# Kernel tuning notes

Hardware: AMD Instinct MI355X
Metric: run time of the kernel (lower is better)

Reference implementation:

```python
import jax, jax.numpy as jnp
import numpy as np

BN_EPS = 1e-5


def setup_inputs() -> dict:
    key = jax.random.key(0)
    ks = jax.random.split(key, 6)
    N, C, T, V = 64, 64, 300, 25
    num_A, O = 3, 64
    x = jax.random.normal(ks[0], (N, C, T, V), dtype=jnp.float32)
    A = jax.random.uniform(ks[1], (num_A, V, V), dtype=jnp.float32)
    # 1x1 conv weights per adjacency branch: W[a, o, c], bias b[a, o]
    W = jax.random.normal(ks[2], (num_A, O, C), dtype=jnp.float32) * (1.0 / np.sqrt(C))
    b = jax.random.normal(ks[3], (num_A, O), dtype=jnp.float32) * 0.01
    gamma = jnp.ones((O,), dtype=jnp.float32)
    beta = jnp.zeros((O,), dtype=jnp.float32)
    return {"x": x, "A": A, "W": W, "b": b, "gamma": gamma, "beta": beta}


def reference(x, A, W, b, gamma, beta):
    # x: [N, C, T, V]; A: [num_A, V, V]; W: [num_A, O, C]; b: [num_A, O]
    # For each branch a: xa = x @ A_a over the joint dim V, then a 1x1 conv
    # (channel mix W_a + bias b_a), accumulated over branches.
    z = jnp.einsum('nctv,avw->anctw', x, A)          # [num_A, N, C, T, V]
    y = jnp.einsum('anctw,aoc->notw', z, W)          # [N, O, T, V]
    y = y + jnp.sum(b, axis=0)[None, :, None, None]
    # BatchNorm2d (training mode: batch statistics over N, T, V per channel)
    mean = jnp.mean(y, axis=(0, 2, 3), keepdims=True)
    var = jnp.mean((y - mean) ** 2, axis=(0, 2, 3), keepdims=True)
    y = (y - mean) * jax.lax.rsqrt(var + BN_EPS)
    y = y * gamma[None, :, None, None] + beta[None, :, None, None]
    return jax.nn.relu(y)
```

## Files before the change

### kernel.cpp

```cpp
#include <hip/hip_runtime.h>


typedef __attribute__((ext_vector_type(8))) short short8;
typedef __attribute__((ext_vector_type(4))) float f32x4;

static __device__ __forceinline__ float bf2f(unsigned short u) {
    return __uint_as_float(((unsigned)u) << 16);
}
static __device__ __forceinline__ unsigned short f2bf(float f) {
    unsigned u = __float_as_uint(f);
    u += 0x7FFFu + ((u >> 16) & 1u);
    return (unsigned short)(u >> 16);
}

#define MFMA16(a, b, c) __builtin_amdgcn_mfma_f32_16x16x32_bf16((a), (b), (c), 0, 0, 0)

__global__ __launch_bounds__(256, 4)
void gcn_k1(const void* __restrict__ xg, const void* __restrict__ Ag,
            const void* __restrict__ Wg, const void* __restrict__ gammag,
            float* __restrict__ gstats, unsigned short* __restrict__ y_ws)
{
    const int tid  = threadIdx.x;
    const int wv   = tid >> 6;
    const int lane = tid & 63;
    const int n16  = lane & 15;
    const int kg   = lane >> 4;
    const int bx   = blockIdx.x;
    const int nb   = bx / 75;
    const int tile = bx - nb * 75;

    const bool isbf = (*(const unsigned*)gammag) == 0x3F803F80u;

    __shared__ __align__(16) unsigned short xs2[256 * 32];
    __shared__ __align__(16) unsigned short AsT[3 * 32 * 32];
    __shared__ __align__(16) unsigned short zsT[112 * 68];
    __shared__ float red[128];

    if (tid < 128) red[tid] = 0.f;

    short8 wfrag[3][2];
    #pragma unroll
    for (int a = 0; a < 3; ++a)
        #pragma unroll
        for (int k2 = 0; k2 < 2; ++k2) {
            const int off = (a * 64 + wv * 16 + n16) * 64 + k2 * 32 + kg * 8;
            if (isbf) {
                wfrag[a][k2] = *(const short8*)((const unsigned short*)Wg + off);
            } else {
                const float* wp = (const float*)Wg + off;
                const float4 w0 = *(const float4*)wp;
                const float4 w1 = *(const float4*)(wp + 4);
                short8 f;
                f[0] = (short)f2bf(w0.x); f[1] = (short)f2bf(w0.y);
                f[2] = (short)f2bf(w0.z); f[3] = (short)f2bf(w0.w);
                f[4] = (short)f2bf(w1.x); f[5] = (short)f2bf(w1.y);
                f[6] = (short)f2bf(w1.z); f[7] = (short)f2bf(w1.w);
                wfrag[a][k2] = f;
            }
        }

    for (int s = tid; s < 3072; s += 256) {
        const int a = s >> 10, w = (s >> 5) & 31, v = s & 31;
        unsigned short val = 0;
        if (v < 25 && w < 25) {
            const int src = (a * 25 + v) * 25 + w;
            val = isbf ? ((const unsigned short*)Ag)[src] : f2bf(((const float*)Ag)[src]);
        }
        AsT[s] = val;
    }

    {
        #pragma unroll
        for (int vv = 25; vv < 32; ++vv) xs2[tid * 32 + vv] = 0;
    }
    if (isbf) {
        const unsigned* xp = (const unsigned*)xg;
        for (int p = tid; p < 3200; p += 256) {
            const int c = p / 50, pc = p - c * 50;
            const unsigned u = xp[(nb * 64 + c) * 3750 + tile * 50 + pc];
            const int r0 = pc * 2, r1 = r0 + 1;
            const int dt0 = r0 / 25, v0 = r0 - dt0 * 25;
            const int dt1 = r1 / 25, v1 = r1 - dt1 * 25;
            xs2[(c * 4 + dt0) * 32 + v0] = (unsigned short)(u & 0xFFFFu);
            xs2[(c * 4 + dt1) * 32 + v1] = (unsigned short)(u >> 16);
        }
    } else {
        const float2* xp = (const float2*)xg;
        for (int p = tid; p < 3200; p += 256) {
            const int c = p / 50, pc = p - c * 50;
            const float2 f = xp[(nb * 64 + c) * 3750 + tile * 50 + pc];
            const int r0 = pc * 2, r1 = r0 + 1;
            const int dt0 = r0 / 25, v0 = r0 - dt0 * 25;
            const int dt1 = r1 / 25, v1 = r1 - dt1 * 25;
            xs2[(c * 4 + dt0) * 32 + v0] = f2bf(f.x);
            xs2[(c * 4 + dt1) * 32 + v1] = f2bf(f.y);
        }
    }

    __syncthreads();

    f32x4 acc[7];
    #pragma unroll
    for (int mt = 0; mt < 7; ++mt) acc[mt] = (f32x4){0.f, 0.f, 0.f, 0.f};

    const f32x4 zero4 = (f32x4){0.f, 0.f, 0.f, 0.f};

    #pragma unroll
    for (int a = 0; a < 3; ++a) {
        const short8 bA0 = *(const short8*)&AsT[(a * 32 +      n16) * 32 + kg * 8];
        const short8 bA1 = *(const short8*)&AsT[(a * 32 + 16 + n16) * 32 + kg * 8];
        f32x4 d[4][2];
        #pragma unroll
        for (int mt = 0; mt < 4; ++mt) {
            const short8 af = *(const short8*)&xs2[(wv * 64 + mt * 16 + n16) * 32 + kg * 8];
            d[mt][0] = MFMA16(af, bA0, zero4);
            d[mt][1] = MFMA16(af, bA1, zero4);
        }
        #pragma unroll
        for (int mt = 0; mt < 4; ++mt) {
            const int c = 16 * wv + mt * 4 + kg;
            #pragma unroll
            for (int r = 0; r < 4; ++r) {
                const int w0 = n16;
                zsT[(r * 25 + w0) * 68 + c] = f2bf(d[mt][0][r]);
                const int w1 = 16 + n16;
                if (w1 < 25) zsT[(r * 25 + w1) * 68 + c] = f2bf(d[mt][1][r]);
            }
        }
        __syncthreads();

        #pragma unroll
        for (int mt = 0; mt < 7; ++mt) {
            #pragma unroll
            for (int k2 = 0; k2 < 2; ++k2) {
                const unsigned short* zp = &zsT[(mt * 16 + n16) * 68 + k2 * 32 + kg * 8];
                const ushort4 z0 = *(const ushort4*)zp;
                const ushort4 z1 = *(const ushort4*)(zp + 4);
                short8 bf;
                bf[0] = (short)z0.x; bf[1] = (short)z0.y; bf[2] = (short)z0.z; bf[3] = (short)z0.w;
                bf[4] = (short)z1.x; bf[5] = (short)z1.y; bf[6] = (short)z1.z; bf[7] = (short)z1.w;
                acc[mt] = MFMA16(wfrag[a][k2], bf, acc[mt]);
            }
        }
        __syncthreads();
    }

    #pragma unroll
    for (int r = 0; r < 4; ++r) {
        const int o = 16 * wv + kg * 4 + r;
        const unsigned rowbase = (unsigned)(nb * 64 + o) * 7500u + (unsigned)tile * 100u;
        float s = 0.f, q = 0.f;
        #pragma unroll
        for (int mt = 0; mt < 7; ++mt) {
            const float v = acc[mt][r];
            const bool valid = (mt < 6) | (n16 < 4);
            const float vm = valid ? v : 0.f;
            s += vm; q += vm * vm;
            const float vhi = __shfl_xor(v, 1);
            if (((n16 & 1) == 0) && valid) {
                const unsigned idx = rowbase + (unsigned)(mt * 16 + n16);
                *(unsigned*)(y_ws + idx) = (unsigned)f2bf(v) | ((unsigned)f2bf(vhi) << 16);
            }
        }
        #pragma unroll
        for (int off = 1; off < 16; off <<= 1) {
            s += __shfl_xor(s, off);
            q += __shfl_xor(q, off);
        }
        if (n16 == 0) { atomicAdd(&red[o], s); atomicAdd(&red[64 + o], q); }
    }

    __syncthreads();
    if (tid < 128) atomicAdd(&gstats[tid], red[tid]);
}

__global__ __launch_bounds__(256)
void gcn_k2(const float* __restrict__ gstats, const unsigned* __restrict__ y32,
            const void* __restrict__ gammag, const void* __restrict__ betag,
            void* __restrict__ outg)
{
    __shared__ float sc[64], sh[64];
    const int tid = threadIdx.x;
    const bool isbf = (*(const unsigned*)gammag) == 0x3F803F80u;

    if (tid < 64) {
        const float inv  = 1.0f / 480000.0f;
        const float mean = gstats[tid] * inv;
        const float var  = gstats[64 + tid] * inv - mean * mean;
        const float rstd = rsqrtf(var + 1e-5f);
        float g, be;
        if (isbf) { g = bf2f(((const unsigned short*)gammag)[tid]); be = bf2f(((const unsigned short*)betag)[tid]); }
        else      { g = ((const float*)gammag)[tid];                be = ((const float*)betag)[tid]; }
        sc[tid] = g * rstd;
        sh[tid] = be - mean * g * rstd;
    }
    __syncthreads();

    const unsigned i = blockIdx.x * 256u + (unsigned)tid;
    const uint4 u = ((const uint4*)y32)[i];
    const unsigned b = i * 4u;
    unsigned wv[4] = {u.x, u.y, u.z, u.w};
    float res[8];
    #pragma unroll
    for (int j = 0; j < 4; ++j) {
        const unsigned o = ((b + j) / 3750u) & 63u;
        const float scl = sc[o], shf = sh[o];
        const float v0 = bf2f((unsigned short)(wv[j] & 0xFFFFu));
        const float v1 = bf2f((unsigned short)(wv[j] >> 16));
        res[2 * j]     = fmaxf(fmaf(v0, scl, shf), 0.f);
        res[2 * j + 1] = fmaxf(fmaf(v1, scl, shf), 0.f);
    }
    if (isbf) {
        uint4 outp;
        outp.x = (unsigned)f2bf(res[0]) | ((unsigned)f2bf(res[1]) << 16);
        outp.y = (unsigned)f2bf(res[2]) | ((unsigned)f2bf(res[3]) << 16);
        outp.z = (unsigned)f2bf(res[4]) | ((unsigned)f2bf(res[5]) << 16);
        outp.w = (unsigned)f2bf(res[6]) | ((unsigned)f2bf(res[7]) << 16);
        ((uint4*)outg)[i] = outp;
    } else {
        float4 f0 = make_float4(res[0], res[1], res[2], res[3]);
        float4 f1 = make_float4(res[4], res[5], res[6], res[7]);
        ((float4*)outg)[2 * i]     = f0;
        ((float4*)outg)[2 * i + 1] = f1;
    }
}

extern "C" void kernel_launch(void* const* d_in, const int* in_sizes, int n_in,
                              void* d_out, int out_size, void* d_ws, size_t ws_size,
                              hipStream_t stream)
{
    (void)in_sizes; (void)n_in; (void)out_size; (void)ws_size;
    const void* x     = d_in[0];
    const void* A     = d_in[1];
    const void* W     = d_in[2];
    const void* gamma = d_in[4];
    const void* beta  = d_in[5];

    float*          gstats = (float*)d_ws;
    unsigned short* y_ws   = (unsigned short*)d_ws + 256;

    hipMemsetAsync(d_ws, 0, 512, stream);
    gcn_k1<<<dim3(64 * 75), dim3(256), 0, stream>>>(x, A, W, gamma, gstats, y_ws);
    gcn_k2<<<dim3(15000), dim3(256), 0, stream>>>(gstats, (const unsigned*)y_ws, gamma, beta, d_out);
}
```

Before: 378.1 us.

## Fuse stats and BN apply into one persistent kernel with grid barrier

Merges the GEMM/statistics kernel and the normalize kernel into one launch of 960 blocks. Each block loops over 5 time tiles, prefetches the next x tile into registers, uses an XOR-swizzled z layout in shared memory, and accumulates statistics across its tiles. A global atomic barrier then lets each block normalize its own y slice. This removes a kernel launch and the tail between the two kernels. The barrier assumes all 960 blocks are resident at once, so it deadlocks if occupancy falls short.

```diff
diff --git a/kernel.cpp b/kernel.cpp
--- a/kernel.cpp
+++ b/kernel.cpp
@@ -3,6 +3,9 @@
 
 typedef __attribute__((ext_vector_type(8))) short short8;
 typedef __attribute__((ext_vector_type(4))) float f32x4;
+
+#define NTILE 5
+#define NBLK  (64 * 15)
 
 static __device__ __forceinline__ float bf2f(unsigned short u) {
     return __uint_as_float(((unsigned)u) << 16);
@@ -12,13 +15,22 @@
     u += 0x7FFFu + ((u >> 16) & 1u);
     return (unsigned short)(u >> 16);
 }
+static __device__ __forceinline__ unsigned pack2bf(float a, float b) {
+    return (unsigned)f2bf(a) | ((unsigned)f2bf(b) << 16);
+}
 
 #define MFMA16(a, b, c) __builtin_amdgcn_mfma_f32_16x16x32_bf16((a), (b), (c), 0, 0, 0)
 
+static __device__ __forceinline__ int zbyte(int m2, int h) {
+    return (m2 * 128 + h * 2) ^ ((m2 & 7) << 4);
+}
+
 __global__ __launch_bounds__(256, 4)
-void gcn_k1(const void* __restrict__ xg, const void* __restrict__ Ag,
-            const void* __restrict__ Wg, const void* __restrict__ gammag,
-            float* __restrict__ gstats, unsigned short* __restrict__ y_ws)
+void gcn_fused(const void* __restrict__ xg, const void* __restrict__ Ag,
+               const void* __restrict__ Wg, const void* __restrict__ gammag,
+               const void* __restrict__ betag,
+               float* __restrict__ gstats, unsigned* __restrict__ bar,
+               unsigned short* __restrict__ y_ws, void* __restrict__ outg)
 {
     const int tid  = threadIdx.x;
     const int wv   = tid >> 6;
@@ -26,17 +38,18 @@
     const int n16  = lane & 15;
     const int kg   = lane >> 4;
     const int bx   = blockIdx.x;
-    const int nb   = bx / 75;
-    const int tile = bx - nb * 75;
+    const int nb   = bx / 15;
+    const int tb   = bx - nb * 15;
 
     const bool isbf = (*(const unsigned*)gammag) == 0x3F803F80u;
 
     __shared__ __align__(16) unsigned short xs2[256 * 32];
     __shared__ __align__(16) unsigned short AsT[3 * 32 * 32];
-    __shared__ __align__(16) unsigned short zsT[112 * 68];
+    __shared__ __align__(16) unsigned short zsT[112 * 64];
     __shared__ float red[128];
 
     if (tid < 128) red[tid] = 0.f;
+    for (int s = tid; s < 12 * 64; s += 256) zsT[100 * 64 + s] = 0;
 
     short8 wfrag[3][2];
     #pragma unroll
@@ -69,159 +82,181 @@
         AsT[s] = val;
     }
 
-    {
-        #pragma unroll
-        for (int vv = 25; vv < 32; ++vv) xs2[tid * 32 + vv] = 0;
-    }
+    #pragma unroll
+    for (int vv = 25; vv < 32; ++vv) xs2[tid * 32 + vv] = 0;
+
+    unsigned px[13];
+    const unsigned* xp32 = (const unsigned*)xg;
     if (isbf) {
-        const unsigned* xp = (const unsigned*)xg;
-        for (int p = tid; p < 3200; p += 256) {
-            const int c = p / 50, pc = p - c * 50;
-            const unsigned u = xp[(nb * 64 + c) * 3750 + tile * 50 + pc];
-            const int r0 = pc * 2, r1 = r0 + 1;
-            const int dt0 = r0 / 25, v0 = r0 - dt0 * 25;
-            const int dt1 = r1 / 25, v1 = r1 - dt1 * 25;
-            xs2[(c * 4 + dt0) * 32 + v0] = (unsigned short)(u & 0xFFFFu);
-            xs2[(c * 4 + dt1) * 32 + v1] = (unsigned short)(u >> 16);
-        }
-    } else {
-        const float2* xp = (const float2*)xg;
-        for (int p = tid; p < 3200; p += 256) {
-            const int c = p / 50, pc = p - c * 50;
-            const float2 f = xp[(nb * 64 + c) * 3750 + tile * 50 + pc];
-            const int r0 = pc * 2, r1 = r0 + 1;
-            const int dt0 = r0 / 25, v0 = r0 - dt0 * 25;
-            const int dt1 = r1 / 25, v1 = r1 - dt1 * 25;
-            xs2[(c * 4 + dt0) * 32 + v0] = f2bf(f.x);
-            xs2[(c * 4 + dt1) * 32 + v1] = f2bf(f.y);
-        }
-    }
-
-    __syncthreads();
+        #pragma unroll
+        for (int j = 0; j < 13; ++j) {
+            const int p = tid + j * 256;
+            if (p < 3200) {
+                const int c = p / 50, pc = p - c * 50;
+                px[j] = xp32[(nb * 64 + c) * 3750 + (tb * 5) * 50 + pc];
+            }
+        }
+    }
 
     f32x4 acc[7];
-    #pragma unroll
-    for (int mt = 0; mt < 7; ++mt) acc[mt] = (f32x4){0.f, 0.f, 0.f, 0.f};
-
     const f32x4 zero4 = (f32x4){0.f, 0.f, 0.f, 0.f};
-
-    #pragma unroll
-    for (int a = 0; a < 3; ++a) {
-        const short8 bA0 = *(const short8*)&AsT[(a * 32 +      n16) * 32 + kg * 8];
-        const short8 bA1 = *(const short8*)&AsT[(a * 32 + 16 + n16) * 32 + kg * 8];
-        f32x4 d[4][2];
-        #pragma unroll
-        for (int mt = 0; mt < 4; ++mt) {
-            const short8 af = *(const short8*)&xs2[(wv * 64 + mt * 16 + n16) * 32 + kg * 8];
-            d[mt][0] = MFMA16(af, bA0, zero4);
-            d[mt][1] = MFMA16(af, bA1, zero4);
-        }
-        #pragma unroll
-        for (int mt = 0; mt < 4; ++mt) {
-            const int c = 16 * wv + mt * 4 + kg;
-            #pragma unroll
-            for (int r = 0; r < 4; ++r) {
-                const int w0 = n16;
-                zsT[(r * 25 + w0) * 68 + c] = f2bf(d[mt][0][r]);
-                const int w1 = 16 + n16;
-                if (w1 < 25) zsT[(r * 25 + w1) * 68 + c] = f2bf(d[mt][1][r]);
+    #pragma unroll
+    for (int mt = 0; mt < 7; ++mt) acc[mt] = zero4;
+    float sacc[4] = {0.f, 0.f, 0.f, 0.f};
+    float qacc[4] = {0.f, 0.f, 0.f, 0.f};
+
+    for (int it = 0; it < NTILE; ++it) {
+        const int t5 = tb * 5 + it;
+
+        if (isbf) {
+            #pragma unroll
+            for (int j = 0; j < 13; ++j) {
+                const int p = tid + j * 256;
+                if (p < 3200) {
+                    const int c = p / 50, pc = p - c * 50;
+                    const unsigned u = px[j];
+                    const int r0 = pc * 2, r1 = r0 + 1;
+                    const int dt0 = r0 / 25, v0 = r0 - dt0 * 25;
+                    const int dt1 = r1 / 25, v1 = r1 - dt1 * 25;
+                    xs2[(dt0 * 64 + c) * 32 + v0] = (unsigned short)(u & 0xFFFFu);
+                    xs2[(dt1 * 64 + c) * 32 + v1] = (unsigned short)(u >> 16);
+                }
+            }
+            if (it + 1 < NTILE) {
+                #pragma unroll
+                for (int j = 0; j < 13; ++j) {
+                    const int p = tid + j * 256;
+                    if (p < 3200) {
+                        const int c = p / 50, pc = p - c * 50;
+                        px[j] = xp32[(nb * 64 + c) * 3750 + (t5 + 1) * 50 + pc];
+                    }
+                }
+            }
+        } else {
+            const float2* xpf = (const float2*)xg;
+            for (int p = tid; p < 3200; p += 256) {
+                const int c = p / 50, pc = p - c * 50;
+                const float2 f = xpf[(nb * 64 + c) * 3750 + t5 * 50 + pc];
+                const int r0 = pc * 2, r1 = r0 + 1;
+                const int dt0 = r0 / 25, v0 = r0 - dt0 * 25;
+                const int dt1 = r1 / 25, v1 = r1 - dt1 * 25;
+                xs2[(dt0 * 64 + c) * 32 + v0] = f2bf(f.x);
+                xs2[(dt1 * 64 + c) * 32 + v1] = f2bf(f.y);
             }
         }
         __syncthreads();
 
         #pragma unroll
-        for (int mt = 0; mt < 7; ++mt) {
-            #pragma unroll
-            for (int k2 = 0; k2 < 2; ++k2) {
-                const unsigned short* zp = &zsT[(mt * 16 + n16) * 68 + k2 * 32 + kg * 8];
-                const ushort4 z0 = *(const ushort4*)zp;
-                const ushort4 z1 = *(const ushort4*)(zp + 4);
-                short8 bf;
-                bf[0] = (short)z0.x; bf[1] = (short)z0.y; bf[2] = (short)z0.z; bf[3] = (short)z0.w;
-                bf[4] = (short)z1.x; bf[5] = (short)z1.y; bf[6] = (short)z1.z; bf[7] = (short)z1.w;
-                acc[mt] = MFMA16(wfrag[a][k2], bf, acc[mt]);
-            }
-        }
-        __syncthreads();
+        for (int a = 0; a < 3; ++a) {
+            const short8 bA0 = *(const short8*)&AsT[(a * 32 +      n16) * 32 + kg * 8];
+            const short8 bA1 = *(const short8*)&AsT[(a * 32 + 16 + n16) * 32 + kg * 8];
+            #pragma unroll
+            for (int mt = 0; mt < 4; ++mt) {
+                const short8 af = *(const short8*)&xs2[(wv * 64 + mt * 16 + n16) * 32 + kg * 8];
+                const f32x4 d0 = MFMA16(af, bA0, zero4);
+                const f32x4 d1 = MFMA16(af, bA1, zero4);
+                const int h = mt * 16 + kg * 4;
+                *(uint2*)((char*)zsT + zbyte(wv * 25 + n16, h)) =
+                    make_uint2(pack2bf(d0[0], d0[1]), pack2bf(d0[2], d0[3]));
+                if (n16 < 9)
+                    *(uint2*)((char*)zsT + zbyte(wv * 25 + 16 + n16, h)) =
+                        make_uint2(pack2bf(d1[0], d1[1]), pack2bf(d1[2], d1[3]));
+            }
+            __syncthreads();
+
+            #pragma unroll
+            for (int mt = 0; mt < 7; ++mt) {
+                #pragma unroll
+                for (int k2 = 0; k2 < 2; ++k2) {
+                    const short8 bf = *(const short8*)((char*)zsT +
+                                        zbyte(mt * 16 + n16, k2 * 32 + kg * 8));
+                    acc[mt] = MFMA16(wfrag[a][k2], bf, acc[mt]);
+                }
+            }
+            __syncthreads();
+        }
+
+        #pragma unroll
+        for (int r = 0; r < 4; ++r) {
+            const int o = 16 * wv + kg * 4 + r;
+            const unsigned rowbase = (unsigned)(nb * 64 + o) * 7500u + (unsigned)t5 * 100u;
+            float s = 0.f, q = 0.f;
+            #pragma unroll
+            for (int mt = 0; mt < 7; ++mt) {
+                const float v = acc[mt][r];
+                const bool valid = (mt < 6) | (n16 < 4);
+                const float vm = valid ? v : 0.f;
+                s += vm; q += vm * vm;
+                const float vhi = __shfl_xor(v, 1);
+                if (((n16 & 1) == 0) && valid)
+                    *(unsigned*)(y_ws + rowbase + (unsigned)(mt * 16 + n16)) = pack2bf(v, vhi);
+            }
+            sacc[r] += s; qacc[r] += q;
+        }
+        #pragma unroll
+        for (int mt = 0; mt < 7; ++mt) acc[mt] = zero4;
     }
 
     #pragma unroll
     for (int r = 0; r < 4; ++r) {
-        const int o = 16 * wv + kg * 4 + r;
-        const unsigned rowbase = (unsigned)(nb * 64 + o) * 7500u + (unsigned)tile * 100u;
-        float s = 0.f, q = 0.f;
-        #pragma unroll
-        for (int mt = 0; mt < 7; ++mt) {
-            const float v = acc[mt][r];
-            const bool valid = (mt < 6) | (n16 < 4);
-            const float vm = valid ? v : 0.f;
-            s += vm; q += vm * vm;
-            const float vhi = __shfl_xor(v, 1);
-            if (((n16 & 1) == 0) && valid) {
-                const unsigned idx = rowbase + (unsigned)(mt * 16 + n16);
-                *(unsigned*)(y_ws + idx) = (unsigned)f2bf(v) | ((unsigned)f2bf(vhi) << 16);
-            }
-        }
+        float s = sacc[r], q = qacc[r];
         #pragma unroll
         for (int off = 1; off < 16; off <<= 1) {
             s += __shfl_xor(s, off);
             q += __shfl_xor(q, off);
         }
-        if (n16 == 0) { atomicAdd(&red[o], s); atomicAdd(&red[64 + o], q); }
-    }
-
+        if (n16 == 0) {
+            const int o = 16 * wv + kg * 4 + r;
+            atomicAdd(&red[o], s);
+            atomicAdd(&red[64 + o], q);
+        }
+    }
     __syncthreads();
     if (tid < 128) atomicAdd(&gstats[tid], red[tid]);
-}
-
-__global__ __launch_bounds__(256)
-void gcn_k2(const float* __restrict__ gstats, const unsigned* __restrict__ y32,
-            const void* __restrict__ gammag, const void* __restrict__ betag,
-            void* __restrict__ outg)
-{
-    __shared__ float sc[64], sh[64];
-    const int tid = threadIdx.x;
-    const bool isbf = (*(const unsigned*)gammag) == 0x3F803F80u;
-
+
+    __syncthreads();
+    if (tid == 0) {
+        __hip_atomic_fetch_add(bar, 1u, __ATOMIC_ACQ_REL, __HIP_MEMORY_SCOPE_AGENT);
+        while (__hip_atomic_load(bar, __ATOMIC_ACQUIRE, __HIP_MEMORY_SCOPE_AGENT) < NBLK)
+            __builtin_amdgcn_s_sleep(2);
+    }
+    __syncthreads();
+
+    if (tid < 128)
+        red[tid] = __hip_atomic_load(&gstats[tid], __ATOMIC_RELAXED, __HIP_MEMORY_SCOPE_AGENT);
+    __syncthreads();
     if (tid < 64) {
         const float inv  = 1.0f / 480000.0f;
-        const float mean = gstats[tid] * inv;
-        const float var  = gstats[64 + tid] * inv - mean * mean;
+        const float mean = red[tid] * inv;
+        const float var  = red[64 + tid] * inv - mean * mean;
         const float rstd = rsqrtf(var + 1e-5f);
         float g, be;
         if (isbf) { g = bf2f(((const unsigned short*)gammag)[tid]); be = bf2f(((const unsigned short*)betag)[tid]); }
         else      { g = ((const float*)gammag)[tid];                be = ((const float*)betag)[tid]; }
-        sc[tid] = g * rstd;
-        sh[tid] = be - mean * g * rstd;
-    }
-    __syncthreads();
-
-    const unsigned i = blockIdx.x * 256u + (unsigned)tid;
-    const uint4 u = ((const uint4*)y32)[i];
-    const unsigned b = i * 4u;
-    unsigned wv[4] = {u.x, u.y, u.z, u.w};
-    float res[8];
-    #pragma unroll
-    for (int j = 0; j < 4; ++j) {
-        const unsigned o = ((b + j) / 3750u) & 63u;
-        const float scl = sc[o], shf = sh[o];
-        const float v0 = bf2f((unsigned short)(wv[j] & 0xFFFFu));
-        const float v1 = bf2f((unsigned short)(wv[j] >> 16));
-        res[2 * j]     = fmaxf(fmaf(v0, scl, shf), 0.f);
-        res[2 * j + 1] = fmaxf(fmaf(v1, scl, shf), 0.f);
-    }
-    if (isbf) {
-        uint4 outp;
-        outp.x = (unsigned)f2bf(res[0]) | ((unsigned)f2bf(res[1]) << 16);
-        outp.y = (unsigned)f2bf(res[2]) | ((unsigned)f2bf(res[3]) << 16);
-        outp.z = (unsigned)f2bf(res[4]) | ((unsigned)f2bf(res[5]) << 16);
-        outp.w = (unsigned)f2bf(res[6]) | ((unsigned)f2bf(res[7]) << 16);
-        ((uint4*)outg)[i] = outp;
-    } else {
-        float4 f0 = make_float4(res[0], res[1], res[2], res[3]);
-        float4 f1 = make_float4(res[4], res[5], res[6], res[7]);
-        ((float4*)outg)[2 * i]     = f0;
-        ((float4*)outg)[2 * i + 1] = f1;
+        red[tid]      = g * rstd;
+        red[64 + tid] = be - mean * g * rstd;
+    }
+    __syncthreads();
+
+    const unsigned* y32 = (const unsigned*)y_ws;
+    for (int s = tid; s < 8000; s += 256) {
+        const int itt = s / 1600;
+        const int rem = s - itt * 1600;
+        const int o   = rem / 25;
+        const int p2  = rem - o * 25;
+        const unsigned a2 = (unsigned)(nb * 64 + o) * 1875u
+                          + (unsigned)(tb * 5 + itt) * 25u + (unsigned)p2;
+        const uint2 u = *(const uint2*)(y32 + 2u * a2);
+        const float scl = red[o], shf = red[64 + o];
+        const float r0 = fmaxf(fmaf(bf2f((unsigned short)(u.x & 0xFFFFu)), scl, shf), 0.f);
+        const float r1 = fmaxf(fmaf(bf2f((unsigned short)(u.x >> 16)),     scl, shf), 0.f);
+        const float r2 = fmaxf(fmaf(bf2f((unsigned short)(u.y & 0xFFFFu)), scl, shf), 0.f);
+        const float r3 = fmaxf(fmaf(bf2f((unsigned short)(u.y >> 16)),     scl, shf), 0.f);
+        if (isbf) {
+            ((uint2*)outg)[a2] = make_uint2(pack2bf(r0, r1), pack2bf(r2, r3));
+        } else {
+            ((float4*)outg)[a2] = make_float4(r0, r1, r2, r3);
+        }
     }
 }
 
@@ -237,9 +272,10 @@
     const void* beta  = d_in[5];
 
     float*          gstats = (float*)d_ws;
-    unsigned short* y_ws   = (unsigned short*)d_ws + 256;
-
-    hipMemsetAsync(d_ws, 0, 512, stream);
-    gcn_k1<<<dim3(64 * 75), dim3(256), 0, stream>>>(x, A, W, gamma, gstats, y_ws);
-    gcn_k2<<<dim3(15000), dim3(256), 0, stream>>>(gstats, (const unsigned*)y_ws, gamma, beta, d_out);
-}
+    unsigned*       bar    = (unsigned*)((char*)d_ws + 512);
+    unsigned short* y_ws   = (unsigned short*)((char*)d_ws + 1024);
+
+    hipMemsetAsync(d_ws, 0, 1024, stream);
+    gcn_fused<<<dim3(NBLK), dim3(256), 0, stream>>>(x, A, W, gamma, beta,
+                                                    gstats, bar, y_ws, d_out);
+}
```

Result: slower. 504.8 us (+33.5%).

## Relayout x and z shared tiles so z is written and read with vector accesses

Applied to the files above, without the earlier changes.

Reorders the x tile in shared memory to be time-major (dt*64+c) so each wave owns one time step, which lets the first MFMA's outputs be packed and stored to zsT as 8-byte vector writes instead of scalar 2-byte scatters. The zsT row stride goes from 68 to 72 so that 16-byte short8 loads are aligned in the second GEMM, and the padding rows are zeroed once up front. The x fragments are also hoisted out of the adjacency loop and reused across all three branches. The cost is a little more shared memory and a different bank-conflict pattern.

```diff
diff --git a/kernel.cpp b/kernel.cpp
--- a/kernel.cpp
+++ b/kernel.cpp
@@ -12,8 +12,13 @@
     u += 0x7FFFu + ((u >> 16) & 1u);
     return (unsigned short)(u >> 16);
 }
+static __device__ __forceinline__ unsigned pack2bf(float a, float b) {
+    return (unsigned)f2bf(a) | ((unsigned)f2bf(b) << 16);
+}
 
 #define MFMA16(a, b, c) __builtin_amdgcn_mfma_f32_16x16x32_bf16((a), (b), (c), 0, 0, 0)
+
+#define ZSTRIDE 72
 
 __global__ __launch_bounds__(256, 4)
 void gcn_k1(const void* __restrict__ xg, const void* __restrict__ Ag,
@@ -33,10 +38,11 @@
 
     __shared__ __align__(16) unsigned short xs2[256 * 32];
     __shared__ __align__(16) unsigned short AsT[3 * 32 * 32];
-    __shared__ __align__(16) unsigned short zsT[112 * 68];
+    __shared__ __align__(16) unsigned short zsT[112 * ZSTRIDE];
     __shared__ float red[128];
 
     if (tid < 128) red[tid] = 0.f;
+    for (int s = tid; s < 12 * ZSTRIDE; s += 256) zsT[100 * ZSTRIDE + s] = 0;
 
     short8 wfrag[3][2];
     #pragma unroll
@@ -81,8 +87,8 @@
             const int r0 = pc * 2, r1 = r0 + 1;
             const int dt0 = r0 / 25, v0 = r0 - dt0 * 25;
             const int dt1 = r1 / 25, v1 = r1 - dt1 * 25;
-            xs2[(c * 4 + dt0) * 32 + v0] = (unsigned short)(u & 0xFFFFu);
-            xs2[(c * 4 + dt1) * 32 + v1] = (unsigned short)(u >> 16);
+            xs2[(dt0 * 64 + c) * 32 + v0] = (unsigned short)(u & 0xFFFFu);
+            xs2[(dt1 * 64 + c) * 32 + v1] = (unsigned short)(u >> 16);
         }
     } else {
         const float2* xp = (const float2*)xg;
@@ -92,40 +98,37 @@
             const int r0 = pc * 2, r1 = r0 + 1;
             const int dt0 = r0 / 25, v0 = r0 - dt0 * 25;
             const int dt1 = r1 / 25, v1 = r1 - dt1 * 25;
-            xs2[(c * 4 + dt0) * 32 + v0] = f2bf(f.x);
-            xs2[(c * 4 + dt1) * 32 + v1] = f2bf(f.y);
+            xs2[(dt0 * 64 + c) * 32 + v0] = f2bf(f.x);
+            xs2[(dt1 * 64 + c) * 32 + v1] = f2bf(f.y);
         }
     }
 
     __syncthreads();
 
+    short8 af[4];
+    #pragma unroll
+    for (int mt = 0; mt < 4; ++mt)
+        af[mt] = *(const short8*)&xs2[(wv * 64 + mt * 16 + n16) * 32 + kg * 8];
+
     f32x4 acc[7];
-    #pragma unroll
-    for (int mt = 0; mt < 7; ++mt) acc[mt] = (f32x4){0.f, 0.f, 0.f, 0.f};
-
     const f32x4 zero4 = (f32x4){0.f, 0.f, 0.f, 0.f};
+    #pragma unroll
+    for (int mt = 0; mt < 7; ++mt) acc[mt] = zero4;
 
     #pragma unroll
     for (int a = 0; a < 3; ++a) {
         const short8 bA0 = *(const short8*)&AsT[(a * 32 +      n16) * 32 + kg * 8];
         const short8 bA1 = *(const short8*)&AsT[(a * 32 + 16 + n16) * 32 + kg * 8];
-        f32x4 d[4][2];
         #pragma unroll
         for (int mt = 0; mt < 4; ++mt) {
-            const short8 af = *(const short8*)&xs2[(wv * 64 + mt * 16 + n16) * 32 + kg * 8];
-            d[mt][0] = MFMA16(af, bA0, zero4);
-            d[mt][1] = MFMA16(af, bA1, zero4);
-        }
-        #pragma unroll
-        for (int mt = 0; mt < 4; ++mt) {
-            const int c = 16 * wv + mt * 4 + kg;
-            #pragma unroll
-            for (int r = 0; r < 4; ++r) {
-                const int w0 = n16;
-                zsT[(r * 25 + w0) * 68 + c] = f2bf(d[mt][0][r]);
-                const int w1 = 16 + n16;
-                if (w1 < 25) zsT[(r * 25 + w1) * 68 + c] = f2bf(d[mt][1][r]);
-            }
+            const f32x4 d0 = MFMA16(af[mt], bA0, zero4);
+            const f32x4 d1 = MFMA16(af[mt], bA1, zero4);
+            const int h = mt * 16 + kg * 4;
+            *(uint2*)&zsT[(wv * 25 + n16) * ZSTRIDE + h] =
+                make_uint2(pack2bf(d0[0], d0[1]), pack2bf(d0[2], d0[3]));
+            if (n16 < 9)
+                *(uint2*)&zsT[(wv * 25 + 16 + n16) * ZSTRIDE + h] =
+                    make_uint2(pack2bf(d1[0], d1[1]), pack2bf(d1[2], d1[3]));
         }
         __syncthreads();
 
@@ -133,12 +136,8 @@
         for (int mt = 0; mt < 7; ++mt) {
             #pragma unroll
             for (int k2 = 0; k2 < 2; ++k2) {
-                const unsigned short* zp = &zsT[(mt * 16 + n16) * 68 + k2 * 32 + kg * 8];
-                const ushort4 z0 = *(const ushort4*)zp;
-                const ushort4 z1 = *(const ushort4*)(zp + 4);
-                short8 bf;
-                bf[0] = (short)z0.x; bf[1] = (short)z0.y; bf[2] = (short)z0.z; bf[3] = (short)z0.w;
-                bf[4] = (short)z1.x; bf[5] = (short)z1.y; bf[6] = (short)z1.z; bf[7] = (short)z1.w;
+                const short8 bf = *(const short8*)&zsT[(mt * 16 + n16) * ZSTRIDE
+                                                       + k2 * 32 + kg * 8];
                 acc[mt] = MFMA16(wfrag[a][k2], bf, acc[mt]);
             }
         }
@@ -157,10 +156,8 @@
             const float vm = valid ? v : 0.f;
             s += vm; q += vm * vm;
             const float vhi = __shfl_xor(v, 1);
-            if (((n16 & 1) == 0) && valid) {
-                const unsigned idx = rowbase + (unsigned)(mt * 16 + n16);
-                *(unsigned*)(y_ws + idx) = (unsigned)f2bf(v) | ((unsigned)f2bf(vhi) << 16);
-            }
+            if (((n16 & 1) == 0) && valid)
+                *(unsigned*)(y_ws + rowbase + (unsigned)(mt * 16 + n16)) = pack2bf(v, vhi);
         }
         #pragma unroll
         for (int off = 1; off < 16; off <<= 1) {
```

After: 377.3 us. About the same (-0.2%).
